# Performance work log

Hardware: AMD Instinct MI355X
Metric: run time of the kernel (lower is better)

## Reference

```python
import jax, jax.numpy as jnp
import numpy as np

BN_EPS = 1e-5


def _batchnorm(x, gamma, beta):
    # training-mode BatchNorm2d: biased batch stats over (N, H, W)
    mean = jnp.mean(x, axis=(0, 2, 3), keepdims=True)
    var = jnp.var(x, axis=(0, 2, 3), keepdims=True)
    xn = (x - mean) * jax.lax.rsqrt(var + BN_EPS)
    return xn * gamma[None, :, None, None] + beta[None, :, None, None]


def _bin_weight(w):
    # BitConv2d_Robust: w_bin = sign(w) * mean(|w|) per output channel (STE in fwd is just the value)
    alpha = jnp.mean(jnp.abs(w), axis=(1, 2, 3), keepdims=True)
    return jax.lax.stop_gradient(jnp.sign(w) * alpha - w) + w


def _conv(x, w, b, pad):
    y = jax.lax.conv_general_dilated(
        x, w, window_strides=(1, 1), padding=[(pad, pad), (pad, pad)],
        dimension_numbers=('NCHW', 'OIHW', 'NCHW'))
    return y + b[None, :, None, None]


def setup_inputs() -> dict:
    key = jax.random.key(0)
    ks = jax.random.split(key, 14)
    B, Cin, Cout, T, H, W = 16, 128, 256, 512, 64, 64
    fan1 = Cin * 9
    fan2 = Cout * 9
    return {
        'x': jax.random.normal(ks[0], (B, Cin, H, W), jnp.float32),
        't': jax.random.normal(ks[1], (B, T), jnp.float32),
        'bn1_g': jnp.ones((Cin,), jnp.float32),
        'bn1_b': jnp.zeros((Cin,), jnp.float32),
        'w1': jax.random.normal(ks[2], (Cout, Cin, 3, 3), jnp.float32) / np.sqrt(fan1),
        'b1': jax.random.normal(ks[3], (Cout,), jnp.float32) * 0.01,
        'tW': jax.random.normal(ks[4], (Cout, T), jnp.float32) / np.sqrt(T),
        'tb': jax.random.normal(ks[5], (Cout,), jnp.float32) * 0.01,
        'bn2_g': jnp.ones((Cout,), jnp.float32),
        'bn2_b': jnp.zeros((Cout,), jnp.float32),
        'w2': jax.random.normal(ks[6], (Cout, Cout, 3, 3), jnp.float32) / np.sqrt(fan2),
        'b2': jax.random.normal(ks[7], (Cout,), jnp.float32) * 0.01,
        'ws': jax.random.normal(ks[8], (Cout, Cin, 1, 1), jnp.float32) / np.sqrt(Cin),
        'bs': jax.random.normal(ks[9], (Cout,), jnp.float32) * 0.01,
    }


def reference(x, t, bn1_g, bn1_b, w1, b1, tW, tb, bn2_g, bn2_b, w2, b2, ws, bs):
    h = jnp.sign(_batchnorm(x, bn1_g, bn1_b))                # BN + sign binarize
    h = _conv(h, _bin_weight(w1), b1, pad=1)                  # binarized 3x3 conv
    temb = t @ tW.T + tb                                      # time MLP -> [B, Cout]
    h = h + temb[:, :, None, None]
    h = jnp.sign(_batchnorm(h, bn2_g, bn2_b))
    h = _conv(h, _bin_weight(w2), b2, pad=1)
    skip = _conv(x, _bin_weight(ws), bs, pad=0)               # 1x1 binarized skip (in_ch != out_ch)
    return h + skip
```

## Files before the change

### kernel.cpp

```cpp
#include <hip/hip_runtime.h>
#include <stdint.h>

typedef unsigned int uint;

#define EPS 1e-5f


__global__ __launch_bounds__(256) void k_bn1_part(const float* __restrict__ x, float* __restrict__ part) {
  int c = blockIdx.x, chunk = blockIdx.y;
  float s = 0.f, s2 = 0.f;
  #pragma unroll
  for (int jb = 0; jb < 2; ++jb) {
    int b = chunk * 2 + jb;
    const float4* xb = (const float4*)(x + (((size_t)((b << 7) | c)) << 12));
    #pragma unroll
    for (int k = 0; k < 4; ++k) {
      float4 q = xb[k * 256 + threadIdx.x];
      s += (q.x + q.y) + (q.z + q.w);
      s2 += q.x * q.x + q.y * q.y + q.z * q.z + q.w * q.w;
    }
  }
  #pragma unroll
  for (int off = 32; off > 0; off >>= 1) { s += __shfl_down(s, off); s2 += __shfl_down(s2, off); }
  __shared__ float ls[4], ls2[4];
  int wid = threadIdx.x >> 6, lane = threadIdx.x & 63;
  if (lane == 0) { ls[wid] = s; ls2[wid] = s2; }
  __syncthreads();
  if (threadIdx.x == 0) {
    part[(c * 8 + chunk) * 2 + 0] = ls[0] + ls[1] + ls[2] + ls[3];
    part[(c * 8 + chunk) * 2 + 1] = ls2[0] + ls2[1] + ls2[2] + ls2[3];
  }
}

__global__ void k_bn1_fin(const float* __restrict__ part, const float* __restrict__ g,
                          const float* __restrict__ be, float* __restrict__ sc, float* __restrict__ sh) {
  int c = threadIdx.x;
  float s = 0.f, s2 = 0.f;
  for (int k = 0; k < 8; ++k) { s += part[(c * 8 + k) * 2]; s2 += part[(c * 8 + k) * 2 + 1]; }
  const float inv = 1.f / 65536.f;
  float m = s * inv, var = s2 * inv - m * m;
  float rs = rsqrtf(var + EPS);
  float scale = rs * g[c];
  sc[c] = scale;
  sh[c] = be[c] - m * scale;
}

__global__ __launch_bounds__(256) void k_bin1(const float* __restrict__ x, const float* __restrict__ sc,
                                              const float* __restrict__ sh, uint2* __restrict__ sbin2) {
  int pg = blockIdx.x * 256 + threadIdx.x;
  int b = pg >> 12, p = pg & 4095;
  int c0 = blockIdx.y << 6;
  const float* xb = x + ((b << 7) << 12) + p;
  uint w[2];
  #pragma unroll
  for (int wd = 0; wd < 2; ++wd) {
    uint acc = 0;
    #pragma unroll
    for (int i = 0; i < 32; ++i) {
      int c = c0 + wd * 32 + i;
      float v = xb[c << 12];
      acc |= ((v * sc[c] + sh[c]) > 0.f ? 1u : 0u) << i;
    }
    w[wd] = acc;
  }
  sbin2[pg * 2 + blockIdx.y] = make_uint2(w[0], w[1]);
}

__global__ __launch_bounds__(128) void k_packw1(const float* __restrict__ w1, uint* __restrict__ wb,
                                                float* __restrict__ alpha) {
  int co = blockIdx.x, wid = threadIdx.x >> 6, lane = threadIdx.x & 63;
  const float* wp = w1 + (co * 128 + threadIdx.x) * 9;
  float wv[9]; float s = 0.f;
  #pragma unroll
  for (int tp = 0; tp < 9; ++tp) { wv[tp] = wp[tp]; s += fabsf(wv[tp]); }
  #pragma unroll
  for (int tp = 0; tp < 9; ++tp) {
    unsigned long long m = __ballot(wv[tp] > 0.f);
    if (lane == 0) {
      wb[(co * 9 + tp) * 4 + wid * 2 + 0] = (uint)m;
      wb[(co * 9 + tp) * 4 + wid * 2 + 1] = (uint)(m >> 32);
    }
  }
  #pragma unroll
  for (int off = 32; off > 0; off >>= 1) s += __shfl_down(s, off);
  __shared__ float l2[2];
  if (lane == 0) l2[wid] = s;
  __syncthreads();
  if (threadIdx.x == 0) alpha[co] = (l2[0] + l2[1]) * (1.f / 1152.f);
}

__global__ __launch_bounds__(256) void k_packw2(const float* __restrict__ w2, uint* __restrict__ wb,
                                                float* __restrict__ alpha) {
  int co = blockIdx.x, wid = threadIdx.x >> 6, lane = threadIdx.x & 63;
  const float* wp = w2 + (co * 256 + threadIdx.x) * 9;
  float wv[9]; float s = 0.f;
  #pragma unroll
  for (int tp = 0; tp < 9; ++tp) { wv[tp] = wp[tp]; s += fabsf(wv[tp]); }
  #pragma unroll
  for (int tp = 0; tp < 9; ++tp) {
    unsigned long long m = __ballot(wv[tp] > 0.f);
    if (lane == 0) {
      wb[(co * 9 + tp) * 8 + wid * 2 + 0] = (uint)m;
      wb[(co * 9 + tp) * 8 + wid * 2 + 1] = (uint)(m >> 32);
    }
  }
  #pragma unroll
  for (int off = 32; off > 0; off >>= 1) s += __shfl_down(s, off);
  __shared__ float l4[4];
  if (lane == 0) l4[wid] = s;
  __syncthreads();
  if (threadIdx.x == 0) alpha[co] = (l4[0] + l4[1] + l4[2] + l4[3]) * (1.f / 2304.f);
}

__global__ __launch_bounds__(256) void k_base(const uint* __restrict__ wb1, const uint* __restrict__ wb2,
                                              int* __restrict__ base1, int* __restrict__ base2) {
  int co = threadIdx.x;
  int pc1[9], pc2[9];
  #pragma unroll
  for (int tp = 0; tp < 9; ++tp) {
    uint a = 0;
    #pragma unroll
    for (int k = 0; k < 4; ++k) a += __popc(wb1[co * 36 + tp * 4 + k]);
    pc1[tp] = (int)a;
    uint b = 0;
    #pragma unroll
    for (int k = 0; k < 8; ++k) b += __popc(wb2[co * 72 + tp * 8 + k]);
    pc2[tp] = (int)b;
  }
  #pragma unroll
  for (int pat = 0; pat < 9; ++pat) {
    int yt = pat / 3, xt = pat % 3;
    int b1v = 1152, b2v = 2304;
    #pragma unroll
    for (int tp = 0; tp < 9; ++tp) {
      int dy = tp / 3 - 1, dx = tp % 3 - 1;
      bool inv = (dy < 0 && yt == 0) || (dy > 0 && yt == 2) || (dx < 0 && xt == 0) || (dx > 0 && xt == 2);
      if (inv) { b1v -= 128 - 2 * pc1[tp]; b2v -= 256 - 2 * pc2[tp]; }
    }
    base1[pat * 256 + co] = b1v;
    base2[pat * 256 + co] = b2v;
  }
}

__global__ __launch_bounds__(128) void k_packws(const float* __restrict__ wsk, float* __restrict__ swT) {
  int co = blockIdx.x, ci = threadIdx.x;
  float v = wsk[co * 128 + ci];
  float s = fabsf(v);
  #pragma unroll
  for (int off = 32; off > 0; off >>= 1) s += __shfl_down(s, off);
  __shared__ float l2[2]; __shared__ float tot;
  int wid = threadIdx.x >> 6, lane = threadIdx.x & 63;
  if (lane == 0) l2[wid] = s;
  __syncthreads();
  if (threadIdx.x == 0) tot = (l2[0] + l2[1]) * (1.f / 128.f);
  __syncthreads();
  float a = tot;
  swT[ci * 256 + co] = (v > 0.f) ? a : -a;
}

__global__ __launch_bounds__(256) void k_temb(const float* __restrict__ t, const float* __restrict__ tW,
                                              const float* __restrict__ tbias, float* __restrict__ temb) {
  int b = blockIdx.x, co = threadIdx.x;
  const float* tr = t + b * 512;
  const float* wr = tW + co * 512;
  float a0 = 0, a1 = 0, a2 = 0, a3 = 0;
  #pragma unroll 8
  for (int k = 0; k < 512; k += 4) {
    a0 = fmaf(tr[k + 0], wr[k + 0], a0);
    a1 = fmaf(tr[k + 1], wr[k + 1], a1);
    a2 = fmaf(tr[k + 2], wr[k + 2], a2);
    a3 = fmaf(tr[k + 3], wr[k + 3], a3);
  }
  temb[b * 256 + co] = (a0 + a1) + (a2 + a3) + tbias[co];
}

__global__ __launch_bounds__(256, 2) void k_conv1(const uint4* __restrict__ sbin, const uint* __restrict__ wb1,
                                                  const int* __restrict__ base1, short* __restrict__ S1) {
  __shared__ uint wlds[32 * 36];
  __shared__ int blds[9 * 32];
  int co0 = blockIdx.y << 5;
  #pragma unroll
  for (int k = 0; k < 4; ++k) wlds[k * 256 + threadIdx.x] = wb1[co0 * 36 + k * 256 + threadIdx.x];
  if (threadIdx.x < 128) wlds[1024 + threadIdx.x] = wb1[co0 * 36 + 1024 + threadIdx.x];
  #pragma unroll
  for (int k = 0; k < 2; ++k) {
    int idx = k * 256 + threadIdx.x;
    if (idx < 288) blds[idx] = base1[(idx >> 5) * 256 + co0 + (idx & 31)];
  }

  int bt = blockIdx.x;
  int b = bt >> 4;
  int y = ((bt & 15) << 2) | (threadIdx.x >> 6);
  int cx = threadIdx.x & 63;
  uint nb[9][4];
  #pragma unroll
  for (int dy = -1; dy <= 1; ++dy)
    #pragma unroll
    for (int dx = -1; dx <= 1; ++dx) {
      int tp = (dy + 1) * 3 + (dx + 1);
      int yy = y + dy, xx = cx + dx;
      bool v = ((unsigned)yy < 64u) && ((unsigned)xx < 64u);
      uint4 q = make_uint4(0, 0, 0, 0);
      if (v) q = sbin[(b << 12) | (yy << 6) | xx];
      nb[tp][0] = q.x; nb[tp][1] = q.y; nb[tp][2] = q.z; nb[tp][3] = q.w;
    }
  int pat = ((y == 0) ? 0 : ((y == 63) ? 6 : 3)) + ((cx == 0) ? 0 : ((cx == 63) ? 2 : 1));
  __syncthreads();

  int p = (y << 6) | cx;
  short* op = S1 + ((size_t)b << 20) + ((size_t)co0 << 12) + p;
  #pragma unroll 1
  for (int cc = 0; cc < 4; ++cc) {
    short accv[8];
    #pragma unroll
    for (int j = 0; j < 8; ++j) {
      int co_l = cc * 8 + j;
      const uint* wp = &wlds[co_l * 36];
      uint m0 = 0, m1 = 0, m2 = 0, m3 = 0;
      #pragma unroll
      for (int tp = 0; tp < 9; ++tp) {
        m0 += __popc(nb[tp][0] ^ wp[tp * 4 + 0]);
        m1 += __popc(nb[tp][1] ^ wp[tp * 4 + 1]);
        m2 += __popc(nb[tp][2] ^ wp[tp * 4 + 2]);
        m3 += __popc(nb[tp][3] ^ wp[tp * 4 + 3]);
      }
      accv[j] = (short)(blds[pat * 32 + co_l] - 2 * (int)((m0 + m1) + (m2 + m3)));
    }
    #pragma unroll
    for (int j = 0; j < 8; ++j) op[(size_t)(cc * 8 + j) << 12] = accv[j];
  }
}

__global__ __launch_bounds__(256) void k_bn2_part(const short* __restrict__ S1, const float* __restrict__ al1,
                                                  const float* __restrict__ b1, const float* __restrict__ temb,
                                                  float* __restrict__ part) {
  int co = blockIdx.x, chunk = blockIdx.y;
  float a = al1[co], bb = b1[co];
  float s = 0.f, s2 = 0.f;
  #pragma unroll
  for (int jb = 0; jb < 2; ++jb) {
    int b = chunk * 2 + jb;
    float tb_ = bb + temb[(b << 8) | co];
    const uint4* sp = (const uint4*)(S1 + ((size_t)b << 20) + ((size_t)co << 12));
    #pragma unroll
    for (int k = 0; k < 2; ++k) {
      uint4 q = sp[k * 256 + threadIdx.x];
      uint ws[4] = {q.x, q.y, q.z, q.w};
      #pragma unroll
      for (int w = 0; w < 4; ++w) {
        float f0 = fmaf(a, (float)((short)(ws[w] & 0xffffu)), tb_);
        float f1 = fmaf(a, (float)((short)(ws[w] >> 16)), tb_);
        s += f0 + f1;
        s2 += f0 * f0 + f1 * f1;
      }
    }
  }
  #pragma unroll
  for (int off = 32; off > 0; off >>= 1) { s += __shfl_down(s, off); s2 += __shfl_down(s2, off); }
  __shared__ float ls[4], ls2[4];
  int wid = threadIdx.x >> 6, lane = threadIdx.x & 63;
  if (lane == 0) { ls[wid] = s; ls2[wid] = s2; }
  __syncthreads();
  if (threadIdx.x == 0) {
    part[(co * 8 + chunk) * 2 + 0] = ls[0] + ls[1] + ls[2] + ls[3];
    part[(co * 8 + chunk) * 2 + 1] = ls2[0] + ls2[1] + ls2[2] + ls2[3];
  }
}

__global__ void k_bn2_fin(const float* __restrict__ part, const float* __restrict__ al1,
                          const float* __restrict__ b1, const float* __restrict__ g2,
                          const float* __restrict__ be2, float* __restrict__ A,
                          float* __restrict__ Bc, float* __restrict__ Cc) {
  int co = threadIdx.x;
  float s = 0.f, s2 = 0.f;
  for (int k = 0; k < 8; ++k) { s += part[(co * 8 + k) * 2]; s2 += part[(co * 8 + k) * 2 + 1]; }
  const float inv = 1.f / 65536.f;
  float m = s * inv, var = s2 * inv - m * m;
  float rs = rsqrtf(var + EPS);
  float gg = rs * g2[co];
  A[co] = al1[co] * gg;
  Bc[co] = (b1[co] - m) * gg + be2[co];
  Cc[co] = gg;
}

__global__ __launch_bounds__(256) void k_bin2(const short* __restrict__ S1, const float* __restrict__ A,
                                              const float* __restrict__ Bc, const float* __restrict__ Cc,
                                              const float* __restrict__ temb, uint4* __restrict__ hbin) {
  int pg = blockIdx.x * 256 + threadIdx.x;
  int b = pg >> 12, p = pg & 4095;
  int c0 = blockIdx.y << 7;
  const short* sp = S1 + ((size_t)b << 20) + p;
  const float* tp = temb + (b << 8);
  uint w[4];
  #pragma unroll
  for (int wd = 0; wd < 4; ++wd) {
    uint acc = 0;
    #pragma unroll
    for (int i = 0; i < 32; ++i) {
      int co = c0 + wd * 32 + i;
      float v = A[co] * (float)sp[(size_t)co << 12] + Bc[co] + Cc[co] * tp[co];
      acc |= (v > 0.f ? 1u : 0u) << i;
    }
    w[wd] = acc;
  }
  hbin[pg * 2 + blockIdx.y] = make_uint4(w[0], w[1], w[2], w[3]);
}

__global__ __launch_bounds__(256, 2) void k_skip(const float* __restrict__ x, const float* __restrict__ swT,
                                                 const float* __restrict__ bsk, const float* __restrict__ b2,
                                                 float* __restrict__ out) {
  __shared__ float xs[128 * 64];
  __shared__ float wsl[128 * 64];
  int g = blockIdx.x;
  int b = g >> 6;
  int px0 = (g & 63) << 6;
  int co0 = blockIdx.y << 6;
  int t = threadIdx.x;

  {
    const float* xb = x + ((size_t)(b << 7) << 12) + px0;
    float4* xs4 = (float4*)xs;
    #pragma unroll
    for (int k = 0; k < 8; ++k) {
      int idx = k * 256 + t;
      int ci = idx >> 4, f4 = idx & 15;
      xs4[idx] = *(const float4*)(xb + ((size_t)ci << 12) + (f4 << 2));
    }
  }
  {
    float4* ws4 = (float4*)wsl;
    #pragma unroll
    for (int k = 0; k < 8; ++k) {
      int idx = k * 256 + t;
      int ci = idx >> 4, f4 = idx & 15;
      ws4[idx] = *(const float4*)(swT + ci * 256 + co0 + (f4 << 2));
    }
  }
  __syncthreads();

  int tx = t & 15, ty = t >> 4;
  const float4* xs4 = (const float4*)xs;
  const float4* ws4 = (const float4*)wsl;
  float4 acc0 = make_float4(0, 0, 0, 0), acc1 = acc0, acc2 = acc0, acc3 = acc0;
  #pragma unroll 4
  for (int ci = 0; ci < 128; ++ci) {
    float4 xv = xs4[ci * 16 + tx];
    float4 wv = ws4[ci * 16 + ty];
    acc0.x = fmaf(wv.x, xv.x, acc0.x); acc0.y = fmaf(wv.x, xv.y, acc0.y);
    acc0.z = fmaf(wv.x, xv.z, acc0.z); acc0.w = fmaf(wv.x, xv.w, acc0.w);
    acc1.x = fmaf(wv.y, xv.x, acc1.x); acc1.y = fmaf(wv.y, xv.y, acc1.y);
    acc1.z = fmaf(wv.y, xv.z, acc1.z); acc1.w = fmaf(wv.y, xv.w, acc1.w);
    acc2.x = fmaf(wv.z, xv.x, acc2.x); acc2.y = fmaf(wv.z, xv.y, acc2.y);
    acc2.z = fmaf(wv.z, xv.z, acc2.z); acc2.w = fmaf(wv.z, xv.w, acc2.w);
    acc3.x = fmaf(wv.w, xv.x, acc3.x); acc3.y = fmaf(wv.w, xv.y, acc3.y);
    acc3.z = fmaf(wv.w, xv.z, acc3.z); acc3.w = fmaf(wv.w, xv.w, acc3.w);
  }

  float* op = out + ((size_t)b << 20) + px0 + (tx << 2);
  int cob = co0 + (ty << 2);
  float4 r;
  r = acc0; { float bb = bsk[cob + 0] + b2[cob + 0]; r.x += bb; r.y += bb; r.z += bb; r.w += bb; }
  *(float4*)(op + (size_t)(cob + 0) * 4096) = r;
  r = acc1; { float bb = bsk[cob + 1] + b2[cob + 1]; r.x += bb; r.y += bb; r.z += bb; r.w += bb; }
  *(float4*)(op + (size_t)(cob + 1) * 4096) = r;
  r = acc2; { float bb = bsk[cob + 2] + b2[cob + 2]; r.x += bb; r.y += bb; r.z += bb; r.w += bb; }
  *(float4*)(op + (size_t)(cob + 2) * 4096) = r;
  r = acc3; { float bb = bsk[cob + 3] + b2[cob + 3]; r.x += bb; r.y += bb; r.z += bb; r.w += bb; }
  *(float4*)(op + (size_t)(cob + 3) * 4096) = r;
}

__global__ __launch_bounds__(256, 2) void k_conv2(const uint4* __restrict__ hbin, const uint* __restrict__ wb2,
                                                  const int* __restrict__ base2, const float* __restrict__ al2,
                                                  float* __restrict__ out) {
  __shared__ uint wlds[32 * 72];
  __shared__ int blds[9 * 32];
  int co0 = blockIdx.y << 5;
  #pragma unroll
  for (int k = 0; k < 9; ++k) wlds[k * 256 + threadIdx.x] = wb2[co0 * 72 + k * 256 + threadIdx.x];
  #pragma unroll
  for (int k = 0; k < 2; ++k) {
    int idx = k * 256 + threadIdx.x;
    if (idx < 288) blds[idx] = base2[(idx >> 5) * 256 + co0 + (idx & 31)];
  }

  int bt = blockIdx.x;
  int b = bt >> 4;
  int y = ((bt & 15) << 2) | (threadIdx.x >> 6);
  int cx = threadIdx.x & 63;
  uint nb[9][8];
  #pragma unroll
  for (int dy = -1; dy <= 1; ++dy)
    #pragma unroll
    for (int dx = -1; dx <= 1; ++dx) {
      int tp = (dy + 1) * 3 + (dx + 1);
      int yy = y + dy, xx = cx + dx;
      bool v = ((unsigned)yy < 64u) && ((unsigned)xx < 64u);
      uint4 q0 = make_uint4(0, 0, 0, 0), q1 = make_uint4(0, 0, 0, 0);
      if (v) {
        int pix = (b << 12) | (yy << 6) | xx;
        q0 = hbin[pix * 2 + 0];
        q1 = hbin[pix * 2 + 1];
      }
      nb[tp][0] = q0.x; nb[tp][1] = q0.y; nb[tp][2] = q0.z; nb[tp][3] = q0.w;
      nb[tp][4] = q1.x; nb[tp][5] = q1.y; nb[tp][6] = q1.z; nb[tp][7] = q1.w;
    }
  int pat = ((y == 0) ? 0 : ((y == 63) ? 6 : 3)) + ((cx == 0) ? 0 : ((cx == 63) ? 2 : 1));
  __syncthreads();

  int p = (y << 6) | cx;
  float* op = out + ((size_t)b << 20) + ((size_t)co0 << 12) + p;
  #pragma unroll 1
  for (int cc = 0; cc < 4; ++cc) {
    float ov[8];
    #pragma unroll
    for (int j = 0; j < 8; ++j) ov[j] = op[(size_t)(cc * 8 + j) << 12];
    #pragma unroll
    for (int j = 0; j < 8; ++j) {
      int co_l = cc * 8 + j;
      const uint* wp = &wlds[co_l * 72];
      uint m0 = 0, m1 = 0, m2 = 0, m3 = 0;
      #pragma unroll
      for (int tp = 0; tp < 9; ++tp) {
        m0 += __popc(nb[tp][0] ^ wp[tp * 8 + 0]);
        m1 += __popc(nb[tp][1] ^ wp[tp * 8 + 1]);
        m2 += __popc(nb[tp][2] ^ wp[tp * 8 + 2]);
        m3 += __popc(nb[tp][3] ^ wp[tp * 8 + 3]);
        m0 += __popc(nb[tp][4] ^ wp[tp * 8 + 4]);
        m1 += __popc(nb[tp][5] ^ wp[tp * 8 + 5]);
        m2 += __popc(nb[tp][6] ^ wp[tp * 8 + 6]);
        m3 += __popc(nb[tp][7] ^ wp[tp * 8 + 7]);
      }
      int acc = blds[pat * 32 + co_l] - 2 * (int)((m0 + m1) + (m2 + m3));
      ov[j] = fmaf(al2[co0 + co_l], (float)acc, ov[j]);
    }
    #pragma unroll
    for (int j = 0; j < 8; ++j) op[(size_t)(cc * 8 + j) << 12] = ov[j];
  }
}

extern "C" void kernel_launch(void* const* d_in, const int* in_sizes, int n_in,
                              void* d_out, int out_size, void* d_ws, size_t ws_size,
                              hipStream_t stream) {
  const float* x    = (const float*)d_in[0];
  const float* t    = (const float*)d_in[1];
  const float* bn1g = (const float*)d_in[2];
  const float* bn1b = (const float*)d_in[3];
  const float* w1   = (const float*)d_in[4];
  const float* b1   = (const float*)d_in[5];
  const float* tW   = (const float*)d_in[6];
  const float* tb   = (const float*)d_in[7];
  const float* bn2g = (const float*)d_in[8];
  const float* bn2b = (const float*)d_in[9];
  const float* w2   = (const float*)d_in[10];
  const float* b2   = (const float*)d_in[11];
  const float* wsk  = (const float*)d_in[12];
  const float* bsk  = (const float*)d_in[13];
  float* out = (float*)d_out;
  char* ws = (char*)d_ws;

  float* bn1part = (float*)(ws + 0);
  float* sc1     = (float*)(ws + 8192);
  float* sh1     = (float*)(ws + 8704);
  uint4* sbin    = (uint4*)(ws + 9216);
  uint*  wb1     = (uint*) (ws + 1057792);
  float* al1     = (float*)(ws + 1094656);
  uint*  wb2     = (uint*) (ws + 1095680);
  float* al2     = (float*)(ws + 1169408);
  float* swkT    = (float*)(ws + 1170432);
  float* temb    = (float*)(ws + 1301504);
  float* bn2part = (float*)(ws + 1317888);
  float* A2      = (float*)(ws + 1334272);
  float* Bc2     = (float*)(ws + 1335296);
  float* Cc2     = (float*)(ws + 1336320);
  uint4* hbin    = (uint4*)(ws + 1337344);
  int*   base1g  = (int*)  (ws + 3434496);
  int*   base2g  = (int*)  (ws + 3443712);
  short* S1      = (short*)(ws + 3452928);

  k_bn1_part<<<dim3(128, 8), 256, 0, stream>>>(x, bn1part);
  k_bn1_fin<<<1, 128, 0, stream>>>(bn1part, bn1g, bn1b, sc1, sh1);
  k_bin1<<<dim3(256, 2), 256, 0, stream>>>(x, sc1, sh1, (uint2*)sbin);
  k_packw1<<<256, 128, 0, stream>>>(w1, wb1, al1);
  k_packw2<<<256, 256, 0, stream>>>(w2, wb2, al2);
  k_base<<<1, 256, 0, stream>>>(wb1, wb2, base1g, base2g);
  k_packws<<<256, 128, 0, stream>>>(wsk, swkT);
  k_temb<<<16, 256, 0, stream>>>(t, tW, tb, temb);
  k_conv1<<<dim3(256, 8), 256, 0, stream>>>(sbin, wb1, base1g, S1);
  k_bn2_part<<<dim3(256, 8), 256, 0, stream>>>(S1, al1, b1, temb, bn2part);
  k_bn2_fin<<<1, 256, 0, stream>>>(bn2part, al1, b1, bn2g, bn2b, A2, Bc2, Cc2);
  k_bin2<<<dim3(256, 2), 256, 0, stream>>>(S1, A2, Bc2, Cc2, temb, hbin);
  k_skip<<<dim3(1024, 4), 256, 0, stream>>>(x, swkT, bsk, b2, out);
  k_conv2<<<dim3(256, 8), 256, 0, stream>>>(hbin, wb2, base2g, al2, out);
}
```

Baseline: 268.3 us.

## Fuse BN1 sign-binarization into skip conv and vectorize LDS weight reads

```diff
diff --git a/kernel.cpp b/kernel.cpp
--- a/kernel.cpp
+++ b/kernel.cpp
@@ -43,27 +43,6 @@
   float scale = rs * g[c];
   sc[c] = scale;
   sh[c] = be[c] - m * scale;
-}
-
-__global__ __launch_bounds__(256) void k_bin1(const float* __restrict__ x, const float* __restrict__ sc,
-                                              const float* __restrict__ sh, uint2* __restrict__ sbin2) {
-  int pg = blockIdx.x * 256 + threadIdx.x;
-  int b = pg >> 12, p = pg & 4095;
-  int c0 = blockIdx.y << 6;
-  const float* xb = x + ((b << 7) << 12) + p;
-  uint w[2];
-  #pragma unroll
-  for (int wd = 0; wd < 2; ++wd) {
-    uint acc = 0;
-    #pragma unroll
-    for (int i = 0; i < 32; ++i) {
-      int c = c0 + wd * 32 + i;
-      float v = xb[c << 12];
-      acc |= ((v * sc[c] + sh[c]) > 0.f ? 1u : 0u) << i;
-    }
-    w[wd] = acc;
-  }
-  sbin2[pg * 2 + blockIdx.y] = make_uint2(w[0], w[1]);
 }
 
 __global__ __launch_bounds__(128) void k_packw1(const float* __restrict__ w1, uint* __restrict__ wb,
@@ -174,141 +153,10 @@
   temb[b * 256 + co] = (a0 + a1) + (a2 + a3) + tbias[co];
 }
 
-__global__ __launch_bounds__(256, 2) void k_conv1(const uint4* __restrict__ sbin, const uint* __restrict__ wb1,
-                                                  const int* __restrict__ base1, short* __restrict__ S1) {
-  __shared__ uint wlds[32 * 36];
-  __shared__ int blds[9 * 32];
-  int co0 = blockIdx.y << 5;
-  #pragma unroll
-  for (int k = 0; k < 4; ++k) wlds[k * 256 + threadIdx.x] = wb1[co0 * 36 + k * 256 + threadIdx.x];
-  if (threadIdx.x < 128) wlds[1024 + threadIdx.x] = wb1[co0 * 36 + 1024 + threadIdx.x];
-  #pragma unroll
-  for (int k = 0; k < 2; ++k) {
-    int idx = k * 256 + threadIdx.x;
-    if (idx < 288) blds[idx] = base1[(idx >> 5) * 256 + co0 + (idx & 31)];
-  }
-
-  int bt = blockIdx.x;
-  int b = bt >> 4;
-  int y = ((bt & 15) << 2) | (threadIdx.x >> 6);
-  int cx = threadIdx.x & 63;
-  uint nb[9][4];
-  #pragma unroll
-  for (int dy = -1; dy <= 1; ++dy)
-    #pragma unroll
-    for (int dx = -1; dx <= 1; ++dx) {
-      int tp = (dy + 1) * 3 + (dx + 1);
-      int yy = y + dy, xx = cx + dx;
-      bool v = ((unsigned)yy < 64u) && ((unsigned)xx < 64u);
-      uint4 q = make_uint4(0, 0, 0, 0);
-      if (v) q = sbin[(b << 12) | (yy << 6) | xx];
-      nb[tp][0] = q.x; nb[tp][1] = q.y; nb[tp][2] = q.z; nb[tp][3] = q.w;
-    }
-  int pat = ((y == 0) ? 0 : ((y == 63) ? 6 : 3)) + ((cx == 0) ? 0 : ((cx == 63) ? 2 : 1));
-  __syncthreads();
-
-  int p = (y << 6) | cx;
-  short* op = S1 + ((size_t)b << 20) + ((size_t)co0 << 12) + p;
-  #pragma unroll 1
-  for (int cc = 0; cc < 4; ++cc) {
-    short accv[8];
-    #pragma unroll
-    for (int j = 0; j < 8; ++j) {
-      int co_l = cc * 8 + j;
-      const uint* wp = &wlds[co_l * 36];
-      uint m0 = 0, m1 = 0, m2 = 0, m3 = 0;
-      #pragma unroll
-      for (int tp = 0; tp < 9; ++tp) {
-        m0 += __popc(nb[tp][0] ^ wp[tp * 4 + 0]);
-        m1 += __popc(nb[tp][1] ^ wp[tp * 4 + 1]);
-        m2 += __popc(nb[tp][2] ^ wp[tp * 4 + 2]);
-        m3 += __popc(nb[tp][3] ^ wp[tp * 4 + 3]);
-      }
-      accv[j] = (short)(blds[pat * 32 + co_l] - 2 * (int)((m0 + m1) + (m2 + m3)));
-    }
-    #pragma unroll
-    for (int j = 0; j < 8; ++j) op[(size_t)(cc * 8 + j) << 12] = accv[j];
-  }
-}
-
-__global__ __launch_bounds__(256) void k_bn2_part(const short* __restrict__ S1, const float* __restrict__ al1,
-                                                  const float* __restrict__ b1, const float* __restrict__ temb,
-                                                  float* __restrict__ part) {
-  int co = blockIdx.x, chunk = blockIdx.y;
-  float a = al1[co], bb = b1[co];
-  float s = 0.f, s2 = 0.f;
-  #pragma unroll
-  for (int jb = 0; jb < 2; ++jb) {
-    int b = chunk * 2 + jb;
-    float tb_ = bb + temb[(b << 8) | co];
-    const uint4* sp = (const uint4*)(S1 + ((size_t)b << 20) + ((size_t)co << 12));
-    #pragma unroll
-    for (int k = 0; k < 2; ++k) {
-      uint4 q = sp[k * 256 + threadIdx.x];
-      uint ws[4] = {q.x, q.y, q.z, q.w};
-      #pragma unroll
-      for (int w = 0; w < 4; ++w) {
-        float f0 = fmaf(a, (float)((short)(ws[w] & 0xffffu)), tb_);
-        float f1 = fmaf(a, (float)((short)(ws[w] >> 16)), tb_);
-        s += f0 + f1;
-        s2 += f0 * f0 + f1 * f1;
-      }
-    }
-  }
-  #pragma unroll
-  for (int off = 32; off > 0; off >>= 1) { s += __shfl_down(s, off); s2 += __shfl_down(s2, off); }
-  __shared__ float ls[4], ls2[4];
-  int wid = threadIdx.x >> 6, lane = threadIdx.x & 63;
-  if (lane == 0) { ls[wid] = s; ls2[wid] = s2; }
-  __syncthreads();
-  if (threadIdx.x == 0) {
-    part[(co * 8 + chunk) * 2 + 0] = ls[0] + ls[1] + ls[2] + ls[3];
-    part[(co * 8 + chunk) * 2 + 1] = ls2[0] + ls2[1] + ls2[2] + ls2[3];
-  }
-}
-
-__global__ void k_bn2_fin(const float* __restrict__ part, const float* __restrict__ al1,
-                          const float* __restrict__ b1, const float* __restrict__ g2,
-                          const float* __restrict__ be2, float* __restrict__ A,
-                          float* __restrict__ Bc, float* __restrict__ Cc) {
-  int co = threadIdx.x;
-  float s = 0.f, s2 = 0.f;
-  for (int k = 0; k < 8; ++k) { s += part[(co * 8 + k) * 2]; s2 += part[(co * 8 + k) * 2 + 1]; }
-  const float inv = 1.f / 65536.f;
-  float m = s * inv, var = s2 * inv - m * m;
-  float rs = rsqrtf(var + EPS);
-  float gg = rs * g2[co];
-  A[co] = al1[co] * gg;
-  Bc[co] = (b1[co] - m) * gg + be2[co];
-  Cc[co] = gg;
-}
-
-__global__ __launch_bounds__(256) void k_bin2(const short* __restrict__ S1, const float* __restrict__ A,
-                                              const float* __restrict__ Bc, const float* __restrict__ Cc,
-                                              const float* __restrict__ temb, uint4* __restrict__ hbin) {
-  int pg = blockIdx.x * 256 + threadIdx.x;
-  int b = pg >> 12, p = pg & 4095;
-  int c0 = blockIdx.y << 7;
-  const short* sp = S1 + ((size_t)b << 20) + p;
-  const float* tp = temb + (b << 8);
-  uint w[4];
-  #pragma unroll
-  for (int wd = 0; wd < 4; ++wd) {
-    uint acc = 0;
-    #pragma unroll
-    for (int i = 0; i < 32; ++i) {
-      int co = c0 + wd * 32 + i;
-      float v = A[co] * (float)sp[(size_t)co << 12] + Bc[co] + Cc[co] * tp[co];
-      acc |= (v > 0.f ? 1u : 0u) << i;
-    }
-    w[wd] = acc;
-  }
-  hbin[pg * 2 + blockIdx.y] = make_uint4(w[0], w[1], w[2], w[3]);
-}
-
 __global__ __launch_bounds__(256, 2) void k_skip(const float* __restrict__ x, const float* __restrict__ swT,
                                                  const float* __restrict__ bsk, const float* __restrict__ b2,
-                                                 float* __restrict__ out) {
+                                                 const float* __restrict__ sc1, const float* __restrict__ sh1,
+                                                 uint* __restrict__ sbinw, float* __restrict__ out) {
   __shared__ float xs[128 * 64];
   __shared__ float wsl[128 * 64];
   int g = blockIdx.x;
@@ -337,6 +185,19 @@
     }
   }
   __syncthreads();
+
+  if (blockIdx.y == 0) {
+    int px = t & 63, wd = t >> 6;
+    int ci0 = wd << 5;
+    uint acc = 0;
+    #pragma unroll
+    for (int i = 0; i < 32; ++i) {
+      int ci = ci0 + i;
+      float v = xs[ci * 64 + px];
+      acc |= ((v * sc1[ci] + sh1[ci]) > 0.f ? 1u : 0u) << i;
+    }
+    sbinw[(((size_t)b << 12) | (px0 + px)) * 4 + wd] = acc;
+  }
 
   int tx = t & 15, ty = t >> 4;
   const float4* xs4 = (const float4*)xs;
@@ -369,7 +230,140 @@
   *(float4*)(op + (size_t)(cob + 3) * 4096) = r;
 }
 
-__global__ __launch_bounds__(256, 2) void k_conv2(const uint4* __restrict__ hbin, const uint* __restrict__ wb2,
+__global__ __launch_bounds__(256, 1) void k_conv1(const uint4* __restrict__ sbin, const uint* __restrict__ wb1,
+                                                  const int* __restrict__ base1, short* __restrict__ S1) {
+  __shared__ uint wlds[32 * 36];
+  __shared__ int blds[9 * 32];
+  int co0 = blockIdx.y << 5;
+  #pragma unroll
+  for (int k = 0; k < 4; ++k) wlds[k * 256 + threadIdx.x] = wb1[co0 * 36 + k * 256 + threadIdx.x];
+  if (threadIdx.x < 128) wlds[1024 + threadIdx.x] = wb1[co0 * 36 + 1024 + threadIdx.x];
+  #pragma unroll
+  for (int k = 0; k < 2; ++k) {
+    int idx = k * 256 + threadIdx.x;
+    if (idx < 288) blds[idx] = base1[(idx >> 5) * 256 + co0 + (idx & 31)];
+  }
+
+  int bt = blockIdx.x;
+  int b = bt >> 4;
+  int y = ((bt & 15) << 2) | (threadIdx.x >> 6);
+  int cx = threadIdx.x & 63;
+  uint nb[9][4];
+  #pragma unroll
+  for (int dy = -1; dy <= 1; ++dy)
+    #pragma unroll
+    for (int dx = -1; dx <= 1; ++dx) {
+      int tp = (dy + 1) * 3 + (dx + 1);
+      int yy = y + dy, xx = cx + dx;
+      bool v = ((unsigned)yy < 64u) && ((unsigned)xx < 64u);
+      uint4 q = make_uint4(0, 0, 0, 0);
+      if (v) q = sbin[(b << 12) | (yy << 6) | xx];
+      nb[tp][0] = q.x; nb[tp][1] = q.y; nb[tp][2] = q.z; nb[tp][3] = q.w;
+    }
+  int pat = ((y == 0) ? 0 : ((y == 63) ? 6 : 3)) + ((cx == 0) ? 0 : ((cx == 63) ? 2 : 1));
+  __syncthreads();
+
+  int p = (y << 6) | cx;
+  short* op = S1 + ((size_t)b << 20) + ((size_t)co0 << 12) + p;
+  #pragma unroll 1
+  for (int cc = 0; cc < 4; ++cc) {
+    short accv[8];
+    #pragma unroll
+    for (int j = 0; j < 8; ++j) {
+      int co_l = cc * 8 + j;
+      const uint4* wp4 = (const uint4*)(wlds + co_l * 36);
+      uint m0 = 0, m1 = 0, m2 = 0, m3 = 0;
+      #pragma unroll
+      for (int tp = 0; tp < 9; ++tp) {
+        uint4 w4 = wp4[tp];
+        m0 += __popc(nb[tp][0] ^ w4.x);
+        m1 += __popc(nb[tp][1] ^ w4.y);
+        m2 += __popc(nb[tp][2] ^ w4.z);
+        m3 += __popc(nb[tp][3] ^ w4.w);
+      }
+      accv[j] = (short)(blds[pat * 32 + co_l] - 2 * (int)((m0 + m1) + (m2 + m3)));
+    }
+    #pragma unroll
+    for (int j = 0; j < 8; ++j) op[(size_t)(cc * 8 + j) << 12] = accv[j];
+  }
+}
+
+__global__ __launch_bounds__(256) void k_bn2_part(const short* __restrict__ S1, const float* __restrict__ al1,
+                                                  const float* __restrict__ b1, const float* __restrict__ temb,
+                                                  float* __restrict__ part) {
+  int co = blockIdx.x, chunk = blockIdx.y;
+  float a = al1[co], bb = b1[co];
+  float s = 0.f, s2 = 0.f;
+  #pragma unroll
+  for (int jb = 0; jb < 2; ++jb) {
+    int b = chunk * 2 + jb;
+    float tb_ = bb + temb[(b << 8) | co];
+    const uint4* sp = (const uint4*)(S1 + ((size_t)b << 20) + ((size_t)co << 12));
+    #pragma unroll
+    for (int k = 0; k < 2; ++k) {
+      uint4 q = sp[k * 256 + threadIdx.x];
+      uint ws[4] = {q.x, q.y, q.z, q.w};
+      #pragma unroll
+      for (int w = 0; w < 4; ++w) {
+        float f0 = fmaf(a, (float)((short)(ws[w] & 0xffffu)), tb_);
+        float f1 = fmaf(a, (float)((short)(ws[w] >> 16)), tb_);
+        s += f0 + f1;
+        s2 += f0 * f0 + f1 * f1;
+      }
+    }
+  }
+  #pragma unroll
+  for (int off = 32; off > 0; off >>= 1) { s += __shfl_down(s, off); s2 += __shfl_down(s2, off); }
+  __shared__ float ls[4], ls2[4];
+  int wid = threadIdx.x >> 6, lane = threadIdx.x & 63;
+  if (lane == 0) { ls[wid] = s; ls2[wid] = s2; }
+  __syncthreads();
+  if (threadIdx.x == 0) {
+    part[(co * 8 + chunk) * 2 + 0] = ls[0] + ls[1] + ls[2] + ls[3];
+    part[(co * 8 + chunk) * 2 + 1] = ls2[0] + ls2[1] + ls2[2] + ls2[3];
+  }
+}
+
+__global__ void k_bn2_fin(const float* __restrict__ part, const float* __restrict__ al1,
+                          const float* __restrict__ b1, const float* __restrict__ g2,
+                          const float* __restrict__ be2, float* __restrict__ A,
+                          float* __restrict__ Bc, float* __restrict__ Cc) {
+  int co = threadIdx.x;
+  float s = 0.f, s2 = 0.f;
+  for (int k = 0; k < 8; ++k) { s += part[(co * 8 + k) * 2]; s2 += part[(co * 8 + k) * 2 + 1]; }
+  const float inv = 1.f / 65536.f;
+  float m = s * inv, var = s2 * inv - m * m;
+  float rs = rsqrtf(var + EPS);
+  float gg = rs * g2[co];
+  A[co] = al1[co] * gg;
+  Bc[co] = (b1[co] - m) * gg + be2[co];
+  Cc[co] = gg;
+}
+
+__global__ __launch_bounds__(256) void k_bin2(const short* __restrict__ S1, const float* __restrict__ A,
+                                              const float* __restrict__ Bc, const float* __restrict__ Cc,
+                                              const float* __restrict__ temb, uint4* __restrict__ hbin) {
+  int pg = blockIdx.x * 256 + threadIdx.x;
+  int b = pg >> 12, p = pg & 4095;
+  int c0 = blockIdx.y << 7;
+  const short* sp = S1 + ((size_t)b << 20) + p;
+  const float* tp = temb + (b << 8);
+  uint w[4];
+  #pragma unroll
+  for (int wd = 0; wd < 4; ++wd) {
+    uint acc = 0;
+    #pragma unroll
+    for (int i = 0; i < 32; ++i) {
+      int co = c0 + wd * 32 + i;
+      float v = A[co] * (float)sp[(size_t)co << 12] + Bc[co] + Cc[co] * tp[co];
+      acc |= (v > 0.f ? 1u : 0u) << i;
+    }
+    w[wd] = acc;
+  }
+  hbin[pg * 2 + blockIdx.y] = make_uint4(w[0], w[1], w[2], w[3]);
+}
+
+__global__ __launch_bounds__(256, 1) void k_conv2(const uint4* __restrict__ hbin, const uint* __restrict__ wb2,
                                                   const int* __restrict__ base2, const float* __restrict__ al2,
                                                   float* __restrict__ out) {
   __shared__ uint wlds[32 * 72];
@@ -417,18 +411,20 @@
     #pragma unroll
     for (int j = 0; j < 8; ++j) {
       int co_l = cc * 8 + j;
-      const uint* wp = &wlds[co_l * 72];
+      const uint4* wp4 = (const uint4*)(wlds + co_l * 72);
       uint m0 = 0, m1 = 0, m2 = 0, m3 = 0;
       #pragma unroll
       for (int tp = 0; tp < 9; ++tp) {
-        m0 += __popc(nb[tp][0] ^ wp[tp * 8 + 0]);
-        m1 += __popc(nb[tp][1] ^ wp[tp * 8 + 1]);
-        m2 += __popc(nb[tp][2] ^ wp[tp * 8 + 2]);
-        m3 += __popc(nb[tp][3] ^ wp[tp * 8 + 3]);
-        m0 += __popc(nb[tp][4] ^ wp[tp * 8 + 4]);
-        m1 += __popc(nb[tp][5] ^ wp[tp * 8 + 5]);
-        m2 += __popc(nb[tp][6] ^ wp[tp * 8 + 6]);
-        m3 += __popc(nb[tp][7] ^ wp[tp * 8 + 7]);
+        uint4 wa = wp4[tp * 2 + 0];
+        uint4 wb_ = wp4[tp * 2 + 1];
+        m0 += __popc(nb[tp][0] ^ wa.x);
+        m1 += __popc(nb[tp][1] ^ wa.y);
+        m2 += __popc(nb[tp][2] ^ wa.z);
+        m3 += __popc(nb[tp][3] ^ wa.w);
+        m0 += __popc(nb[tp][4] ^ wb_.x);
+        m1 += __popc(nb[tp][5] ^ wb_.y);
+        m2 += __popc(nb[tp][6] ^ wb_.z);
+        m3 += __popc(nb[tp][7] ^ wb_.w);
       }
       int acc = blds[pat * 32 + co_l] - 2 * (int)((m0 + m1) + (m2 + m3));
       ov[j] = fmaf(al2[co0 + co_l], (float)acc, ov[j]);
@@ -479,16 +475,15 @@
 
   k_bn1_part<<<dim3(128, 8), 256, 0, stream>>>(x, bn1part);
   k_bn1_fin<<<1, 128, 0, stream>>>(bn1part, bn1g, bn1b, sc1, sh1);
-  k_bin1<<<dim3(256, 2), 256, 0, stream>>>(x, sc1, sh1, (uint2*)sbin);
   k_packw1<<<256, 128, 0, stream>>>(w1, wb1, al1);
   k_packw2<<<256, 256, 0, stream>>>(w2, wb2, al2);
   k_base<<<1, 256, 0, stream>>>(wb1, wb2, base1g, base2g);
   k_packws<<<256, 128, 0, stream>>>(wsk, swkT);
   k_temb<<<16, 256, 0, stream>>>(t, tW, tb, temb);
+  k_skip<<<dim3(1024, 4), 256, 0, stream>>>(x, swkT, bsk, b2, sc1, sh1, (uint*)sbin, out);
   k_conv1<<<dim3(256, 8), 256, 0, stream>>>(sbin, wb1, base1g, S1);
   k_bn2_part<<<dim3(256, 8), 256, 0, stream>>>(S1, al1, b1, temb, bn2part);
   k_bn2_fin<<<1, 256, 0, stream>>>(bn2part, al1, b1, bn2g, bn2b, A2, Bc2, Cc2);
   k_bin2<<<dim3(256, 2), 256, 0, stream>>>(S1, A2, Bc2, Cc2, temb, hbin);
-  k_skip<<<dim3(1024, 4), 256, 0, stream>>>(x, swkT, bsk, b2, out);
   k_conv2<<<dim3(256, 8), 256, 0, stream>>>(hbin, wb2, base2g, al2, out);
 }
```

After: 259.7 us. 3.2% less time.
